# Performance work log

Hardware: AMD Instinct MI355X
Metric: run time of the kernel (lower is better)

## Reference

```python
import jax, jax.numpy as jnp
import numpy as np

B = 16
N = [4096, 1024, 256, 64, 16]
NF = [1, 16, 32, 64, 128, 256]
DEG = 6
KS = 5
LAT = 32


def spline_conv(x, edge_index, pseudo, W, root, bias):
    """SplineConv: open B-spline, degree 1, dim 3, kernel_size 5, sum aggregation (norm=False).
    x: [Nn, Cin], edge_index: [2, E] (src, dst), pseudo: [E, 3] in [0,1], W: [125, Cin, Cout]."""
    src, dst = edge_index[0], edge_index[1]
    v = pseudo * (KS - 1)                       # degree-1 open spline interval
    lo = jnp.clip(jnp.floor(v), 0.0, KS - 2)
    frac = v - lo                               # [E, 3]
    lo = lo.astype(jnp.int32)
    xs = x[src]                                 # [E, Cin] gather
    strides = jnp.array([1, KS, KS * KS], dtype=jnp.int32)
    msg = jnp.zeros((src.shape[0], W.shape[2]), dtype=x.dtype)
    for s in range(8):                          # (degree+1)^dim = 8 basis products
        bits = np.array([(s >> d) & 1 for d in range(3)], dtype=np.int32)
        basis = jnp.prod(jnp.where(bits[None, :] == 1, frac, 1.0 - frac), axis=1)  # [E]
        kidx = jnp.sum((lo + bits[None, :]) * strides[None, :], axis=1)            # [E]
        Wg = W[kidx]                                                               # [E, Cin, Cout]
        msg = msg + basis[:, None] * jnp.einsum('ei,eio->eo', xs, Wg)
    agg = jax.ops.segment_sum(msg, dst, num_segments=x.shape[0])
    return agg + x @ root + bias


def _fwd(fl, ei):
    (x, ea0, ea1, ea2, ea3, ea4, P01, P12, P23, P34, Pn1, P1n, P43, P32, P21, P10,
     W_c1, r_c1, b_c1, W_c2, r_c2, b_c2, W_c3, r_c3, b_c3, W_c4, r_c4, b_c4, W_c5, r_c5, b_c5,
     W_d5, r_d5, b_d5, W_d4, r_d4, b_d4, W_d3, r_d3, b_d3, W_d2, r_d2, b_d2, W_d1, r_d1, b_d1,
     fce1_w, fce1_b, fce21_w, fce21_b, fce22_w, fce22_b, fcd3_w, fcd3_b, fcd4_w, fcd4_b, eps) = fl
    ei0, ei1, ei2, ei3, ei4 = ei
    elu = jax.nn.elu
    # ---- encoder ----
    h = elu(spline_conv(x, ei0, ea0, W_c1, r_c1, b_c1))
    h = P01 @ h.reshape(B, N[0], NF[1])
    h = elu(spline_conv(h.reshape(-1, NF[1]), ei1, ea1, W_c2, r_c2, b_c2))
    h = P12 @ h.reshape(B, N[1], NF[2])
    h = elu(spline_conv(h.reshape(-1, NF[2]), ei2, ea2, W_c3, r_c3, b_c3))
    h = P23 @ h.reshape(B, N[2], NF[3])
    h = elu(spline_conv(h.reshape(-1, NF[3]), ei3, ea3, W_c4, r_c4, b_c4))
    h = P34 @ h.reshape(B, N[3], NF[4])
    h = elu(spline_conv(h.reshape(-1, NF[4]), ei4, ea4, W_c5, r_c5, b_c5))
    h = (Pn1 @ h.reshape(B, N[4], NF[5])).reshape(B, NF[5])
    # 1x1 convs over [B, C, 1, 1] == dense layers
    h = elu(h @ fce1_w + fce1_b)
    mu = h @ fce21_w + fce21_b
    logvar = h @ fce22_w + fce22_b
    # ---- reparameterize ----
    z = eps * jnp.exp(0.5 * logvar) + mu
    # ---- decoder ----
    h = elu(z @ fcd3_w + fcd3_b)
    h = elu(h @ fcd4_w + fcd4_b)
    h = P1n @ h.reshape(B, 1, NF[5])            # [B, N4, nf5]
    h = elu(spline_conv(h.reshape(-1, NF[5]), ei4, ea4, W_d5, r_d5, b_d5))
    h = P43 @ h.reshape(B, N[4], NF[4])
    h = elu(spline_conv(h.reshape(-1, NF[4]), ei3, ea3, W_d4, r_d4, b_d4))
    h = P32 @ h.reshape(B, N[3], NF[3])
    h = elu(spline_conv(h.reshape(-1, NF[3]), ei2, ea2, W_d3, r_d3, b_d3))
    h = P21 @ h.reshape(B, N[2], NF[2])
    h = elu(spline_conv(h.reshape(-1, NF[2]), ei1, ea1, W_d2, r_d2, b_d2))
    h = P10 @ h.reshape(B, N[1], NF[1])
    h = elu(spline_conv(h.reshape(-1, NF[1]), ei0, ea0, W_d1, r_d1, b_d1))
    recon = h.reshape(B, -1)                    # [B, N0] (nf0 == 1)
    return recon, mu, logvar


def setup_inputs() -> dict:
    key = jax.random.key(0)
    ks = iter(jax.random.split(key, 128))
    def nrm(shape, scale=1.0):
        return jax.random.normal(next(ks), shape, dtype=jnp.float32) * scale
    def edges(n):
        # per-sample random mesh-like connectivity, offset per graph copy
        e = jax.random.randint(next(ks), (2, B, n * DEG), 0, n)
        off = (jnp.arange(B) * n)[None, :, None]
        return (e + off).reshape(2, -1).astype(jnp.int32)
    inp = {}
    inp['x'] = nrm((B * N[0], NF[0]))
    for i in range(5):
        inp[f'ea{i}'] = jax.random.uniform(next(ks), (B * N[i] * DEG, 3), dtype=jnp.float32)
    pools = {'P01': (N[1], N[0]), 'P12': (N[2], N[1]), 'P23': (N[3], N[2]), 'P34': (N[4], N[3]),
             'Pn1': (1, N[4]), 'P1n': (N[4], 1), 'P43': (N[3], N[4]), 'P32': (N[2], N[3]),
             'P21': (N[1], N[2]), 'P10': (N[0], N[1])}
    for k2, (a, b) in pools.items():
        inp[k2] = nrm((a, b), 1.0 / np.sqrt(b))
    def spl(name, ci, co):
        inp[f'W_{name}'] = nrm((KS ** 3, ci, co), 0.1 / np.sqrt(ci))
        inp[f'r_{name}'] = nrm((ci, co), 1.0 / np.sqrt(ci))
        inp[f'b_{name}'] = nrm((co,), 0.01)
    spl('c1', NF[0], NF[1]); spl('c2', NF[1], NF[2]); spl('c3', NF[2], NF[3]); spl('c4', NF[3], NF[4]); spl('c5', NF[4], NF[5])
    spl('d5', NF[5], NF[4]); spl('d4', NF[4], NF[3]); spl('d3', NF[3], NF[2]); spl('d2', NF[2], NF[1]); spl('d1', NF[1], NF[0])
    def lin(name, ci, co):
        inp[f'{name}_w'] = nrm((ci, co), 1.0 / np.sqrt(ci))
        inp[f'{name}_b'] = nrm((co,), 0.01)
    lin('fce1', NF[5], NF[5]); lin('fce21', NF[5], LAT); lin('fce22', NF[5], LAT)
    lin('fcd3', LAT, NF[5]); lin('fcd4', NF[5], NF[5])
    inp['eps'] = nrm((B, LAT))
    for i in range(5):
        inp[f'ei{i}'] = edges(N[i])
    return inp


def reference(x, ea0, ea1, ea2, ea3, ea4, P01, P12, P23, P34, Pn1, P1n, P43, P32, P21, P10,
              W_c1, r_c1, b_c1, W_c2, r_c2, b_c2, W_c3, r_c3, b_c3, W_c4, r_c4, b_c4, W_c5, r_c5, b_c5,
              W_d5, r_d5, b_d5, W_d4, r_d4, b_d4, W_d3, r_d3, b_d3, W_d2, r_d2, b_d2, W_d1, r_d1, b_d1,
              fce1_w, fce1_b, fce21_w, fce21_b, fce22_w, fce22_b, fcd3_w, fcd3_b, fcd4_w, fcd4_b, eps,
              ei0, ei1, ei2, ei3, ei4):
    fl = (x, ea0, ea1, ea2, ea3, ea4, P01, P12, P23, P34, Pn1, P1n, P43, P32, P21, P10,
          W_c1, r_c1, b_c1, W_c2, r_c2, b_c2, W_c3, r_c3, b_c3, W_c4, r_c4, b_c4, W_c5, r_c5, b_c5,
          W_d5, r_d5, b_d5, W_d4, r_d4, b_d4, W_d3, r_d3, b_d3, W_d2, r_d2, b_d2, W_d1, r_d1, b_d1,
          fce1_w, fce1_b, fce21_w, fce21_b, fce22_w, fce22_b, fcd3_w, fcd3_b, fcd4_w, fcd4_b, eps)
    return _fwd(fl, (ei0, ei1, ei2, ei3, ei4))
```

## Files before the change

### kernel.cpp

```cpp
#include <hip/hip_runtime.h>
#include <hip/hip_bf16.h>

#define TPB 256
#define CDIV(a,b) (((a)+(b)-1)/(b))

__device__ __forceinline__ float elu_f(float v) {
    return v > 0.f ? v : expm1f(v);
}

__device__ __forceinline__ int ld_idx(const void* __restrict__ ei, int pos, int is64) {
    if (is64) return (int)((const long long*)ei)[pos];
    return ((const int*)ei)[pos];
}

__global__ void k_detect(const int* __restrict__ ei0_as_i32, int* __restrict__ flag) {
    if (threadIdx.x == 0 && blockIdx.x == 0) {
        int zeros = 0;
        for (int k = 0; k < 128; ++k)
            if (ei0_as_i32[2 * k + 1] == 0) zeros++;
        flag[0] = (zeros >= 120) ? 1 : 0;
    }
}

__global__ __launch_bounds__(TPB) void k_zero(float* __restrict__ p, int n) {
    int t = blockIdx.x * blockDim.x + threadIdx.x;
    if (t < n) p[t] = 0.f;
}

__global__ __launch_bounds__(TPB) void k_root(const float* __restrict__ x,
                                              const float* __restrict__ root,
                                              const float* __restrict__ bias,
                                              float* __restrict__ out,
                                              int nnode, int cin, int cout) {
    int t = blockIdx.x * blockDim.x + threadIdx.x;
    if (t >= nnode * cout) return;
    int n = t / cout, co = t - n * cout;
    const float* xp = x + n * cin;
    float acc = bias[co];
    for (int ci = 0; ci < cin; ++ci) acc = fmaf(xp[ci], root[ci * cout + co], acc);
    out[t] = acc;
}

__global__ __launch_bounds__(TPB) void k_root4(const float* __restrict__ x,
                                               const float* __restrict__ root,
                                               const float* __restrict__ bias,
                                               float* __restrict__ out,
                                               int nnode, int cin, int cout) {
    int t = blockIdx.x * blockDim.x + threadIdx.x;
    if (t >= nnode * cout) return;
    int n = t / cout, co = t - n * cout;
    const float4* xr = reinterpret_cast<const float4*>(x + n * cin);
    float a0 = 0.f, a1 = 0.f, a2 = 0.f, a3 = 0.f;
    int q4 = cin >> 2;
    for (int q = 0; q < q4; ++q) {
        float4 xv = xr[q];
        const float* rp = root + (q * 4) * cout + co;
        a0 = fmaf(xv.x, rp[0], a0);
        a1 = fmaf(xv.y, rp[cout], a1);
        a2 = fmaf(xv.z, rp[2 * cout], a2);
        a3 = fmaf(xv.w, rp[3 * cout], a3);
    }
    out[t] = bias[co] + ((a0 + a1) + (a2 + a3));
}

template <int CIN, int COUT, int CSPLIT>
__global__ __launch_bounds__(TPB) void k_msg4(const float* __restrict__ x,
                                              const float* __restrict__ pseudo,
                                              const void* __restrict__ ei,
                                              const float* __restrict__ W,
                                              float* __restrict__ agg, int E,
                                              const int* __restrict__ flag) {
    constexpr int COG = COUT / 4;
    constexpr int CPT = CIN / CSPLIT;
    int t = blockIdx.x * blockDim.x + threadIdx.x;
    if (t >= E * COG * CSPLIT) return;
    int is64 = flag[0];
    int cog = t % COG;
    int rest = t / COG;
    int cs = rest % CSPLIT;
    int e = rest / CSPLIT;
    int co0 = cog * 4;
    int src = ld_idx(ei, e, is64);
    int dst = ld_idx(ei, E + e, is64);

    float f[3]; int lo[3];
#pragma unroll
    for (int d = 0; d < 3; ++d) {
        float v = pseudo[e * 3 + d] * 4.f;
        float l = floorf(v);
        l = fminf(fmaxf(l, 0.f), 3.f);
        f[d] = v - l;
        lo[d] = (int)l;
    }
    float bas[8]; int wof[8];
#pragma unroll
    for (int s = 0; s < 8; ++s) {
        int b0 = s & 1, b1 = (s >> 1) & 1, b2 = (s >> 2) & 1;
        bas[s] = (b0 ? f[0] : 1.f - f[0]) * (b1 ? f[1] : 1.f - f[1]) * (b2 ? f[2] : 1.f - f[2]);
        int kidx = (lo[0] + b0) + 5 * (lo[1] + b1) + 25 * (lo[2] + b2);
        wof[s] = kidx * CIN * COUT + co0;
    }
    float a0 = 0.f, a1 = 0.f, a2 = 0.f, a3 = 0.f;
    const float* xp = x + src * CIN + cs * CPT;
    const int cbase = cs * CPT * COUT;
    for (int ci = 0; ci < CPT; ++ci) {
        float xv = xp[ci];
        int off = cbase + ci * COUT;
#pragma unroll
        for (int s = 0; s < 8; ++s) {
            float4 w = *reinterpret_cast<const float4*>(&W[wof[s] + off]);
            float bx = bas[s] * xv;
            a0 = fmaf(bx, w.x, a0);
            a1 = fmaf(bx, w.y, a1);
            a2 = fmaf(bx, w.z, a2);
            a3 = fmaf(bx, w.w, a3);
        }
    }
    float* ap = &agg[dst * COUT + co0];
    atomicAdd(ap + 0, a0);
    atomicAdd(ap + 1, a1);
    atomicAdd(ap + 2, a2);
    atomicAdd(ap + 3, a3);
}

template <int CIN, int COUT>
__global__ __launch_bounds__(TPB) void k_msg_s(const float* __restrict__ x,
                                               const float* __restrict__ pseudo,
                                               const void* __restrict__ ei,
                                               const float* __restrict__ W,
                                               float* __restrict__ agg, int E,
                                               const int* __restrict__ flag) {
    int t = blockIdx.x * blockDim.x + threadIdx.x;
    if (t >= E * COUT) return;
    int is64 = flag[0];
    int e = t / COUT, co = t - e * COUT;
    int src = ld_idx(ei, e, is64);
    int dst = ld_idx(ei, E + e, is64);
    float f[3]; int lo[3];
#pragma unroll
    for (int d = 0; d < 3; ++d) {
        float v = pseudo[e * 3 + d] * 4.f;
        float l = floorf(v);
        l = fminf(fmaxf(l, 0.f), 3.f);
        f[d] = v - l;
        lo[d] = (int)l;
    }
    float bas[8]; int wof[8];
#pragma unroll
    for (int s = 0; s < 8; ++s) {
        int b0 = s & 1, b1 = (s >> 1) & 1, b2 = (s >> 2) & 1;
        bas[s] = (b0 ? f[0] : 1.f - f[0]) * (b1 ? f[1] : 1.f - f[1]) * (b2 ? f[2] : 1.f - f[2]);
        int kidx = (lo[0] + b0) + 5 * (lo[1] + b1) + 25 * (lo[2] + b2);
        wof[s] = kidx * CIN * COUT + co;
    }
    float acc = 0.f;
    const float* xp = x + src * CIN;
    for (int ci = 0; ci < CIN; ++ci) {
        float xv = xp[ci];
#pragma unroll
        for (int s = 0; s < 8; ++s) acc = fmaf(bas[s] * xv, W[wof[s] + ci * COUT], acc);
    }
    atomicAdd(&agg[dst * COUT + co], acc);
}

template <int F, int JT, int ELU>
__global__ __launch_bounds__(TPB) void k_pool_t(const float* __restrict__ in,
                                                const float* __restrict__ P,
                                                float* __restrict__ out,
                                                int nout, int nin) {
    constexpr int FQ = F / 4;
    constexpr int IQ = TPB / FQ;
    constexpr int NI = 4;
    constexpr int TI = IQ * NI;
    __shared__ float4 s_in[JT * FQ];
    int fq = threadIdx.x % FQ;
    int iq = threadIdx.x / FQ;
    int b = blockIdx.y;
    int i0 = blockIdx.x * TI + iq * NI;
    int nchunk = nin / gridDim.z;
    int jbeg = blockIdx.z * nchunk;
    const float4* inb4 = reinterpret_cast<const float4*>(in + b * nin * F);

    float4 acc[NI];
#pragma unroll
    for (int n = 0; n < NI; ++n) acc[n] = make_float4(0.f, 0.f, 0.f, 0.f);

    for (int j0 = jbeg; j0 < jbeg + nchunk; j0 += JT) {
        __syncthreads();
        for (int t = threadIdx.x; t < JT * FQ; t += TPB) {
            float4 v = inb4[(j0 + t / FQ) * FQ + (t % FQ)];
            if (ELU) {
                v.x = elu_f(v.x); v.y = elu_f(v.y);
                v.z = elu_f(v.z); v.w = elu_f(v.w);
            }
            s_in[t] = v;
        }
        __syncthreads();
#pragma unroll 2
        for (int j = 0; j < JT; j += 4) {
            float4 v0 = s_in[(j + 0) * FQ + fq];
            float4 v1 = s_in[(j + 1) * FQ + fq];
            float4 v2 = s_in[(j + 2) * FQ + fq];
            float4 v3 = s_in[(j + 3) * FQ + fq];
#pragma unroll
            for (int n = 0; n < NI; ++n) {
                float4 pv = *reinterpret_cast<const float4*>(&P[(i0 + n) * nin + j0 + j]);
                acc[n].x = fmaf(pv.x, v0.x, acc[n].x); acc[n].y = fmaf(pv.x, v0.y, acc[n].y);
                acc[n].z = fmaf(pv.x, v0.z, acc[n].z); acc[n].w = fmaf(pv.x, v0.w, acc[n].w);
                acc[n].x = fmaf(pv.y, v1.x, acc[n].x); acc[n].y = fmaf(pv.y, v1.y, acc[n].y);
                acc[n].z = fmaf(pv.y, v1.z, acc[n].z); acc[n].w = fmaf(pv.y, v1.w, acc[n].w);
                acc[n].x = fmaf(pv.z, v2.x, acc[n].x); acc[n].y = fmaf(pv.z, v2.y, acc[n].y);
                acc[n].z = fmaf(pv.z, v2.z, acc[n].z); acc[n].w = fmaf(pv.z, v2.w, acc[n].w);
                acc[n].x = fmaf(pv.w, v3.x, acc[n].x); acc[n].y = fmaf(pv.w, v3.y, acc[n].y);
                acc[n].z = fmaf(pv.w, v3.z, acc[n].z); acc[n].w = fmaf(pv.w, v3.w, acc[n].w);
            }
        }
    }
#pragma unroll
    for (int n = 0; n < NI; ++n) {
        int i = i0 + n;
        if (i >= nout) continue;
        float* o = out + (b * nout + i) * F + fq * 4;
        if (gridDim.z > 1) {
            atomicAdd(o + 0, acc[n].x); atomicAdd(o + 1, acc[n].y);
            atomicAdd(o + 2, acc[n].z); atomicAdd(o + 3, acc[n].w);
        } else {
            *reinterpret_cast<float4*>(o) = acc[n];
        }
    }
}

__global__ __launch_bounds__(TPB) void k_pool_e(const float* __restrict__ in,
                                                const float* __restrict__ P,
                                                float* __restrict__ out,
                                                int nout, int nin, int F, int elu) {
    int t = blockIdx.x * blockDim.x + threadIdx.x;
    if (t >= 16 * nout * F) return;
    int f = t % F;
    int rest = t / F;
    int i = rest % nout;
    int b = rest / nout;
    const float* ip = in + b * nin * F + f;
    const float* pp = P + i * nin;
    float acc = 0.f;
    if (elu) {
#pragma unroll 4
        for (int j = 0; j < nin; ++j) acc = fmaf(pp[j], elu_f(ip[j * F]), acc);
    } else {
#pragma unroll 4
        for (int j = 0; j < nin; ++j) acc = fmaf(pp[j], ip[j * F], acc);
    }
    out[t] = acc;
}

__global__ __launch_bounds__(256) void k_fc_fused(
        const float* __restrict__ c5agg,
        const float* __restrict__ Pn1,
        const float* __restrict__ fce1_w, const float* __restrict__ fce1_b,
        const float* __restrict__ fce21_w, const float* __restrict__ fce21_b,
        const float* __restrict__ fce22_w, const float* __restrict__ fce22_b,
        const float* __restrict__ eps,
        const float* __restrict__ fcd3_w, const float* __restrict__ fcd3_b,
        const float* __restrict__ fcd4_w, const float* __restrict__ fcd4_b,
        const float* __restrict__ P1n,
        float* __restrict__ out_mu, float* __restrict__ out_lv,
        float* __restrict__ dec_in)
{
    __shared__ float s0[256], s1[256], s2[32];
    int b = blockIdx.x, t = threadIdx.x;

    const float* ap = c5agg + b * 4096 + t;
    float acc = 0.f;
#pragma unroll
    for (int n = 0; n < 16; ++n) acc = fmaf(Pn1[n], elu_f(ap[n * 256]), acc);
    s0[t] = acc;
    __syncthreads();

    float a = fce1_b[t];
    for (int ci = 0; ci < 256; ci += 8) {
#pragma unroll
        for (int k = 0; k < 8; ++k) a = fmaf(s0[ci + k], fce1_w[(ci + k) * 256 + t], a);
    }
    s1[t] = elu_f(a);
    __syncthreads();

    if (t < 64) {
        const float* w  = (t < 32) ? fce21_w : fce22_w;
        const float* bb = (t < 32) ? fce21_b : fce22_b;
        int co = t & 31;
        float m = bb[co];
        for (int ci = 0; ci < 256; ci += 8) {
#pragma unroll
            for (int k = 0; k < 8; ++k) m = fmaf(s1[ci + k], w[(ci + k) * 32 + co], m);
        }
        if (t < 32) { out_mu[b * 32 + co] = m; s2[co] = m; }
        else        { out_lv[b * 32 + co] = m; s0[co] = m; }
    }
    __syncthreads();
    if (t < 32) s2[t] = fmaf(eps[b * 32 + t], expf(0.5f * s0[t]), s2[t]);
    __syncthreads();

    float d = fcd3_b[t];
#pragma unroll
    for (int ci = 0; ci < 32; ++ci) d = fmaf(s2[ci], fcd3_w[ci * 256 + t], d);
    s0[t] = elu_f(d);
    __syncthreads();

    float e = fcd4_b[t];
    for (int ci = 0; ci < 256; ci += 8) {
#pragma unroll
        for (int k = 0; k < 8; ++k) e = fmaf(s0[ci + k], fcd4_w[(ci + k) * 256 + t], e);
    }
    e = elu_f(e);

    float* op = dec_in + b * 4096 + t;
#pragma unroll
    for (int n = 0; n < 16; ++n) op[n * 256] = P1n[n] * e;
}

__global__ __launch_bounds__(TPB) void k_elu_out(const float* __restrict__ in,
                                                 float* __restrict__ out, int n) {
    int t = blockIdx.x * blockDim.x + threadIdx.x;
    if (t < n) out[t] = elu_f(in[t]);
}

extern "C" void kernel_launch(void* const* d_in, const int* in_sizes, int n_in,
                              void* d_out, int out_size, void* d_ws, size_t ws_size,
                              hipStream_t stream) {
    const float* x    = (const float*)d_in[0];
    const float* ea0  = (const float*)d_in[1];
    const float* ea1  = (const float*)d_in[2];
    const float* ea2  = (const float*)d_in[3];
    const float* ea3  = (const float*)d_in[4];
    const float* ea4  = (const float*)d_in[5];
    const float* P01  = (const float*)d_in[6];
    const float* P12  = (const float*)d_in[7];
    const float* P23  = (const float*)d_in[8];
    const float* P34  = (const float*)d_in[9];
    const float* Pn1  = (const float*)d_in[10];
    const float* P1n  = (const float*)d_in[11];
    const float* P43  = (const float*)d_in[12];
    const float* P32  = (const float*)d_in[13];
    const float* P21  = (const float*)d_in[14];
    const float* P10  = (const float*)d_in[15];
    const float* W_c1 = (const float*)d_in[16]; const float* r_c1 = (const float*)d_in[17]; const float* b_c1 = (const float*)d_in[18];
    const float* W_c2 = (const float*)d_in[19]; const float* r_c2 = (const float*)d_in[20]; const float* b_c2 = (const float*)d_in[21];
    const float* W_c3 = (const float*)d_in[22]; const float* r_c3 = (const float*)d_in[23]; const float* b_c3 = (const float*)d_in[24];
    const float* W_c4 = (const float*)d_in[25]; const float* r_c4 = (const float*)d_in[26]; const float* b_c4 = (const float*)d_in[27];
    const float* W_c5 = (const float*)d_in[28]; const float* r_c5 = (const float*)d_in[29]; const float* b_c5 = (const float*)d_in[30];
    const float* W_d5 = (const float*)d_in[31]; const float* r_d5 = (const float*)d_in[32]; const float* b_d5 = (const float*)d_in[33];
    const float* W_d4 = (const float*)d_in[34]; const float* r_d4 = (const float*)d_in[35]; const float* b_d4 = (const float*)d_in[36];
    const float* W_d3 = (const float*)d_in[37]; const float* r_d3 = (const float*)d_in[38]; const float* b_d3 = (const float*)d_in[39];
    const float* W_d2 = (const float*)d_in[40]; const float* r_d2 = (const float*)d_in[41]; const float* b_d2 = (const float*)d_in[42];
    const float* W_d1 = (const float*)d_in[43]; const float* r_d1 = (const float*)d_in[44]; const float* b_d1 = (const float*)d_in[45];
    const float* fce1_w  = (const float*)d_in[46]; const float* fce1_b  = (const float*)d_in[47];
    const float* fce21_w = (const float*)d_in[48]; const float* fce21_b = (const float*)d_in[49];
    const float* fce22_w = (const float*)d_in[50]; const float* fce22_b = (const float*)d_in[51];
    const float* fcd3_w  = (const float*)d_in[52]; const float* fcd3_b  = (const float*)d_in[53];
    const float* fcd4_w  = (const float*)d_in[54]; const float* fcd4_b  = (const float*)d_in[55];
    const float* eps  = (const float*)d_in[56];
    const void* ei0 = d_in[57];
    const void* ei1 = d_in[58];
    const void* ei2 = d_in[59];
    const void* ei3 = d_in[60];
    const void* ei4 = d_in[61];

    const int E0 = 393216, E1 = 98304, E2 = 24576, E3 = 6144, E4 = 1536;
    const int N0 = 65536, N1 = 16384, N2 = 4096, N3 = 1024, N4 = 256;

    float* sm   = (float*)d_ws;
    float* bufA = sm + 13824;
    float* bufB = bufA + 1048576;
    int*  flag  = (int*)(bufB + 262144);

    float* out = (float*)d_out;
    float* out_mu = out + 65536;
    float* out_lv = out + 66048;

    auto g = [](int n) { return dim3((unsigned)CDIV(n, TPB)); };

    k_detect<<<1, 64, 0, stream>>>((const int*)ei0, flag);

    k_root<<<g(N0 * 16), TPB, 0, stream>>>(x, r_c1, b_c1, bufA, N0, 1, 16);
    k_msg4<1, 16, 1><<<g(E0 * 4), TPB, 0, stream>>>(x, ea0, ei0, W_c1, bufA, E0, flag);
    k_zero<<<g(262144), TPB, 0, stream>>>(bufB, 262144);
    k_pool_t<16, 128, 1><<<dim3(4, 16, 4), TPB, 0, stream>>>(bufA, P01, bufB, 1024, 4096);

    k_root4<<<g(N1 * 32), TPB, 0, stream>>>(bufB, r_c2, b_c2, bufA, N1, 16, 32);
    k_msg4<16, 32, 1><<<g(E1 * 8), TPB, 0, stream>>>(bufB, ea1, ei1, W_c2, bufA, E1, flag);
    k_zero<<<g(131072), TPB, 0, stream>>>(bufB, 131072);
    k_pool_t<32, 128, 1><<<dim3(2, 16, 4), TPB, 0, stream>>>(bufA, P12, bufB, 256, 1024);

    k_root4<<<g(N2 * 64), TPB, 0, stream>>>(bufB, r_c3, b_c3, bufA, N2, 32, 64);
    k_msg4<32, 64, 1><<<g(E2 * 16), TPB, 0, stream>>>(bufB, ea2, ei2, W_c3, bufA, E2, flag);
    k_zero<<<g(65536), TPB, 0, stream>>>(bufB, 65536);
    k_pool_t<64, 64, 1><<<dim3(1, 16, 2), TPB, 0, stream>>>(bufA, P23, bufB, 64, 256);

    k_root4<<<g(N3 * 128), TPB, 0, stream>>>(bufB, r_c4, b_c4, bufA, N3, 64, 128);
    k_msg4<64, 128, 1><<<g(E3 * 32), TPB, 0, stream>>>(bufB, ea3, ei3, W_c4, bufA, E3, flag);
    k_pool_e<<<g(16 * 16 * 128), TPB, 0, stream>>>(bufA, P34, bufB, 16, 64, 128, 1);

    k_root4<<<g(N4 * 256), TPB, 0, stream>>>(bufB, r_c5, b_c5, bufA, N4, 128, 256);
    k_msg4<128, 256, 2><<<g(E4 * 128), TPB, 0, stream>>>(bufB, ea4, ei4, W_c5, bufA, E4, flag);

    k_fc_fused<<<16, 256, 0, stream>>>(bufA, Pn1,
                                       fce1_w, fce1_b, fce21_w, fce21_b, fce22_w, fce22_b,
                                       eps, fcd3_w, fcd3_b, fcd4_w, fcd4_b, P1n,
                                       out_mu, out_lv, bufA);

    k_root4<<<g(N4 * 128), TPB, 0, stream>>>(bufA, r_d5, b_d5, bufB, N4, 256, 128);
    k_msg4<256, 128, 4><<<g(E4 * 128), TPB, 0, stream>>>(bufA, ea4, ei4, W_d5, bufB, E4, flag);
    k_pool_e<<<g(16 * 64 * 128), TPB, 0, stream>>>(bufB, P43, bufA, 64, 16, 128, 1);

    k_root4<<<g(N3 * 64), TPB, 0, stream>>>(bufA, r_d4, b_d4, bufB, N3, 128, 64);
    k_msg4<128, 64, 2><<<g(E3 * 32), TPB, 0, stream>>>(bufA, ea3, ei3, W_d4, bufB, E3, flag);
    k_pool_t<64, 64, 1><<<dim3(4, 16, 1), TPB, 0, stream>>>(bufB, P32, bufA, 256, 64);

    k_root4<<<g(N2 * 32), TPB, 0, stream>>>(bufA, r_d3, b_d3, bufB, N2, 64, 32);
    k_msg4<64, 32, 1><<<g(E2 * 8), TPB, 0, stream>>>(bufA, ea2, ei2, W_d3, bufB, E2, flag);
    k_zero<<<g(524288), TPB, 0, stream>>>(bufA, 524288);
    k_pool_t<32, 128, 1><<<dim3(8, 16, 2), TPB, 0, stream>>>(bufB, P21, bufA, 1024, 256);

    k_root4<<<g(N1 * 16), TPB, 0, stream>>>(bufA, r_d2, b_d2, bufB, N1, 32, 16);
    k_msg4<32, 16, 1><<<g(E1 * 4), TPB, 0, stream>>>(bufA, ea1, ei1, W_d2, bufB, E1, flag);
    k_pool_t<16, 128, 1><<<dim3(16, 16, 1), TPB, 0, stream>>>(bufB, P10, bufA, 4096, 1024);

    k_root4<<<g(N0 * 1), TPB, 0, stream>>>(bufA, r_d1, b_d1, bufB, N0, 16, 1);
    k_msg_s<16, 1><<<g(E0 * 1), TPB, 0, stream>>>(bufA, ea0, ei0, W_d1, bufB, E0, flag);
    k_elu_out<<<g(N0), TPB, 0, stream>>>(bufB, out, 65536);
}
```

Before: 1.062 ms.

## Specialize first/last spline convs with shared-memory aggregation and rework pooling and FC kernels

The first encoder conv is replaced by a per-graph kernel that fuses the root/bias term and aggregates messages with shared-memory atomics, using weights cached in LDS. The last decoder conv does the same, writing per-segment partial sums that a finalize kernel reduces together with ELU. The pooling kernels become non-atomic one-output-per-thread GEMVs, which removes the zeroing launches, with an optional split-K path and a reduction step. The FC block moves to 1024 threads with split-K partial sums. Together these cut global atomics, launches and serialized FC work, but they depend on edges being grouped per graph and on a larger workspace being available.

```diff
diff --git a/kernel.cpp b/kernel.cpp
--- a/kernel.cpp
+++ b/kernel.cpp
@@ -11,6 +11,25 @@
 __device__ __forceinline__ int ld_idx(const void* __restrict__ ei, int pos, int is64) {
     if (is64) return (int)((const long long*)ei)[pos];
     return ((const int*)ei)[pos];
+}
+
+__device__ __forceinline__ void spline_basis(const float* __restrict__ pseudo, int e,
+                                             float bas[8], int kidx[8]) {
+    float f[3]; int lo[3];
+#pragma unroll
+    for (int d = 0; d < 3; ++d) {
+        float v = pseudo[e * 3 + d] * 4.f;
+        float l = floorf(v);
+        l = fminf(fmaxf(l, 0.f), 3.f);
+        f[d] = v - l;
+        lo[d] = (int)l;
+    }
+#pragma unroll
+    for (int s = 0; s < 8; ++s) {
+        int b0 = s & 1, b1 = (s >> 1) & 1, b2 = (s >> 2) & 1;
+        bas[s] = (b0 ? f[0] : 1.f - f[0]) * (b1 ? f[1] : 1.f - f[1]) * (b2 ? f[2] : 1.f - f[2]);
+        kidx[s] = (lo[0] + b0) + 5 * (lo[1] + b1) + 25 * (lo[2] + b2);
+    }
 }
 
 __global__ void k_detect(const int* __restrict__ ei0_as_i32, int* __restrict__ flag) {
@@ -25,20 +44,6 @@
 __global__ __launch_bounds__(TPB) void k_zero(float* __restrict__ p, int n) {
     int t = blockIdx.x * blockDim.x + threadIdx.x;
     if (t < n) p[t] = 0.f;
-}
-
-__global__ __launch_bounds__(TPB) void k_root(const float* __restrict__ x,
-                                              const float* __restrict__ root,
-                                              const float* __restrict__ bias,
-                                              float* __restrict__ out,
-                                              int nnode, int cin, int cout) {
-    int t = blockIdx.x * blockDim.x + threadIdx.x;
-    if (t >= nnode * cout) return;
-    int n = t / cout, co = t - n * cout;
-    const float* xp = x + n * cin;
-    float acc = bias[co];
-    for (int ci = 0; ci < cin; ++ci) acc = fmaf(xp[ci], root[ci * cout + co], acc);
-    out[t] = acc;
 }
 
 __global__ __launch_bounds__(TPB) void k_root4(const float* __restrict__ x,
@@ -82,24 +87,11 @@
     int co0 = cog * 4;
     int src = ld_idx(ei, e, is64);
     int dst = ld_idx(ei, E + e, is64);
-
-    float f[3]; int lo[3];
-#pragma unroll
-    for (int d = 0; d < 3; ++d) {
-        float v = pseudo[e * 3 + d] * 4.f;
-        float l = floorf(v);
-        l = fminf(fmaxf(l, 0.f), 3.f);
-        f[d] = v - l;
-        lo[d] = (int)l;
-    }
-    float bas[8]; int wof[8];
-#pragma unroll
-    for (int s = 0; s < 8; ++s) {
-        int b0 = s & 1, b1 = (s >> 1) & 1, b2 = (s >> 2) & 1;
-        bas[s] = (b0 ? f[0] : 1.f - f[0]) * (b1 ? f[1] : 1.f - f[1]) * (b2 ? f[2] : 1.f - f[2]);
-        int kidx = (lo[0] + b0) + 5 * (lo[1] + b1) + 25 * (lo[2] + b2);
-        wof[s] = kidx * CIN * COUT + co0;
-    }
+    float bas[8]; int kidx[8];
+    spline_basis(pseudo, e, bas, kidx);
+    int wof[8];
+#pragma unroll
+    for (int s = 0; s < 8; ++s) wof[s] = kidx[s] * CIN * COUT + co0;
     float a0 = 0.f, a1 = 0.f, a2 = 0.f, a3 = 0.f;
     const float* xp = x + src * CIN + cs * CPT;
     const int cbase = cs * CPT * COUT;
@@ -136,31 +128,176 @@
     int e = t / COUT, co = t - e * COUT;
     int src = ld_idx(ei, e, is64);
     int dst = ld_idx(ei, E + e, is64);
-    float f[3]; int lo[3];
-#pragma unroll
-    for (int d = 0; d < 3; ++d) {
-        float v = pseudo[e * 3 + d] * 4.f;
-        float l = floorf(v);
-        l = fminf(fmaxf(l, 0.f), 3.f);
-        f[d] = v - l;
-        lo[d] = (int)l;
-    }
-    float bas[8]; int wof[8];
-#pragma unroll
-    for (int s = 0; s < 8; ++s) {
-        int b0 = s & 1, b1 = (s >> 1) & 1, b2 = (s >> 2) & 1;
-        bas[s] = (b0 ? f[0] : 1.f - f[0]) * (b1 ? f[1] : 1.f - f[1]) * (b2 ? f[2] : 1.f - f[2]);
-        int kidx = (lo[0] + b0) + 5 * (lo[1] + b1) + 25 * (lo[2] + b2);
-        wof[s] = kidx * CIN * COUT + co;
-    }
+    float bas[8]; int kidx[8];
+    spline_basis(pseudo, e, bas, kidx);
     float acc = 0.f;
     const float* xp = x + src * CIN;
     for (int ci = 0; ci < CIN; ++ci) {
         float xv = xp[ci];
 #pragma unroll
-        for (int s = 0; s < 8; ++s) acc = fmaf(bas[s] * xv, W[wof[s] + ci * COUT], acc);
+        for (int s = 0; s < 8; ++s)
+            acc = fmaf(bas[s] * xv, W[kidx[s] * CIN * COUT + ci * COUT + co], acc);
     }
     atomicAdd(&agg[dst * COUT + co], acc);
+}
+
+__global__ __launch_bounds__(1024) void k_msg_c1(const float* __restrict__ x,
+                                                 const float* __restrict__ pseudo,
+                                                 const void* __restrict__ ei,
+                                                 const float* __restrict__ W,
+                                                 const float* __restrict__ root,
+                                                 const float* __restrict__ bias,
+                                                 float* __restrict__ agg,
+                                                 const int* __restrict__ flag) {
+    __shared__ float s_acc[4096 * 4];
+    __shared__ float s_w[125 * 4];
+    int b = blockIdx.x, cg = blockIdx.y, t = threadIdx.x;
+    int co0 = cg * 4;
+    int is64 = flag[0];
+    if (t < 500) s_w[t] = W[(t >> 2) * 16 + co0 + (t & 3)];
+    float r0 = root[co0], r1 = root[co0 + 1], r2 = root[co0 + 2], r3 = root[co0 + 3];
+    float b0 = bias[co0], b1 = bias[co0 + 1], b2 = bias[co0 + 2], b3 = bias[co0 + 3];
+    for (int n = t; n < 4096; n += 1024) {
+        float xv = x[b * 4096 + n];
+        s_acc[n * 4 + 0] = fmaf(xv, r0, b0);
+        s_acc[n * 4 + 1] = fmaf(xv, r1, b1);
+        s_acc[n * 4 + 2] = fmaf(xv, r2, b2);
+        s_acc[n * 4 + 3] = fmaf(xv, r3, b3);
+    }
+    __syncthreads();
+    int ebeg = b * 24576;
+    for (int k = t; k < 24576; k += 1024) {
+        int e = ebeg + k;
+        int src = ld_idx(ei, e, is64);
+        int dst = ld_idx(ei, 393216 + e, is64);
+        float xv = x[src];
+        float bas[8]; int kidx[8];
+        spline_basis(pseudo, e, bas, kidx);
+        float m0 = 0.f, m1 = 0.f, m2 = 0.f, m3 = 0.f;
+#pragma unroll
+        for (int s = 0; s < 8; ++s) {
+            const float* wp = s_w + kidx[s] * 4;
+            float bs = bas[s];
+            m0 = fmaf(bs, wp[0], m0);
+            m1 = fmaf(bs, wp[1], m1);
+            m2 = fmaf(bs, wp[2], m2);
+            m3 = fmaf(bs, wp[3], m3);
+        }
+        int dl = (dst - b * 4096) * 4;
+        atomicAdd(&s_acc[dl + 0], m0 * xv);
+        atomicAdd(&s_acc[dl + 1], m1 * xv);
+        atomicAdd(&s_acc[dl + 2], m2 * xv);
+        atomicAdd(&s_acc[dl + 3], m3 * xv);
+    }
+    __syncthreads();
+    for (int n = t; n < 4096; n += 1024) {
+        float4 v = *reinterpret_cast<float4*>(&s_acc[n * 4]);
+        *reinterpret_cast<float4*>(&agg[(b * 4096 + n) * 16 + co0]) = v;
+    }
+}
+
+__global__ __launch_bounds__(512) void k_msg_d1(const float* __restrict__ x,
+                                                const float* __restrict__ pseudo,
+                                                const void* __restrict__ ei,
+                                                const float* __restrict__ W,
+                                                float* __restrict__ part,
+                                                const int* __restrict__ flag) {
+    __shared__ float s_acc[4096];
+    __shared__ float s_w[2000];
+    int b = blockIdx.x, seg = blockIdx.y, t = threadIdx.x;
+    int is64 = flag[0];
+    for (int i = t; i < 2000; i += 512) s_w[i] = W[i];
+    for (int n = t; n < 4096; n += 512) s_acc[n] = 0.f;
+    __syncthreads();
+    int ebeg = b * 24576 + seg * 3072;
+    for (int k = t; k < 3072; k += 512) {
+        int e = ebeg + k;
+        int src = ld_idx(ei, e, is64);
+        int dst = ld_idx(ei, 393216 + e, is64);
+        float bas[8]; int kidx[8];
+        spline_basis(pseudo, e, bas, kidx);
+        const float* xp = x + src * 16;
+        float m = 0.f;
+#pragma unroll
+        for (int s = 0; s < 8; ++s) {
+            const float* wp = s_w + kidx[s] * 16;
+            float p = 0.f;
+#pragma unroll
+            for (int ci = 0; ci < 16; ++ci) p = fmaf(xp[ci], wp[ci], p);
+            m = fmaf(bas[s], p, m);
+        }
+        atomicAdd(&s_acc[dst - b * 4096], m);
+    }
+    __syncthreads();
+    for (int n = t; n < 4096; n += 512) part[(b * 8 + seg) * 4096 + n] = s_acc[n];
+}
+
+__global__ __launch_bounds__(TPB) void k_d1_fin(const float* __restrict__ root,
+                                                const float* __restrict__ part,
+                                                float* __restrict__ out) {
+    int t = blockIdx.x * blockDim.x + threadIdx.x;
+    if (t >= 65536) return;
+    int b = t >> 12, n = t & 4095;
+    float a = root[t];
+#pragma unroll
+    for (int s = 0; s < 8; ++s) a += part[(b * 8 + s) * 4096 + n];
+    out[t] = elu_f(a);
+}
+
+template <int F, int ELU>
+__global__ __launch_bounds__(256) void k_poolg(const float* __restrict__ in,
+                                               const float* __restrict__ P,
+                                               float* __restrict__ out,
+                                               int nout, int nin) {
+    constexpr int FQ = F / 4;
+    constexpr int TI = 256 / FQ;
+    constexpr int JT = 128;
+    __shared__ float4 s_in[JT * FQ];
+    int fq = threadIdx.x % FQ;
+    int i = threadIdx.x / FQ;
+    int b = blockIdx.y;
+    int gi = blockIdx.x * TI + i;
+    int nchunk = nin / gridDim.z;
+    int jbeg = blockIdx.z * nchunk;
+    const float4* inb4 = reinterpret_cast<const float4*>(in + b * nin * F);
+    const float* prow = P + gi * nin;
+    float4 acc = make_float4(0.f, 0.f, 0.f, 0.f);
+    for (int j0 = jbeg; j0 < jbeg + nchunk; j0 += JT) {
+        __syncthreads();
+        for (int t = threadIdx.x; t < JT * FQ; t += 256) {
+            float4 v = inb4[(j0 + t / FQ) * FQ + (t % FQ)];
+            if (ELU) {
+                v.x = elu_f(v.x); v.y = elu_f(v.y);
+                v.z = elu_f(v.z); v.w = elu_f(v.w);
+            }
+            s_in[t] = v;
+        }
+        __syncthreads();
+#pragma unroll 4
+        for (int j = 0; j < JT; j += 4) {
+            float4 pv = *reinterpret_cast<const float4*>(prow + j0 + j);
+            float4 v0 = s_in[(j + 0) * FQ + fq];
+            float4 v1 = s_in[(j + 1) * FQ + fq];
+            float4 v2 = s_in[(j + 2) * FQ + fq];
+            float4 v3 = s_in[(j + 3) * FQ + fq];
+            acc.x = fmaf(pv.x, v0.x, acc.x); acc.y = fmaf(pv.x, v0.y, acc.y);
+            acc.z = fmaf(pv.x, v0.z, acc.z); acc.w = fmaf(pv.x, v0.w, acc.w);
+            acc.x = fmaf(pv.y, v1.x, acc.x); acc.y = fmaf(pv.y, v1.y, acc.y);
+            acc.z = fmaf(pv.y, v1.z, acc.z); acc.w = fmaf(pv.y, v1.w, acc.w);
+            acc.x = fmaf(pv.z, v2.x, acc.x); acc.y = fmaf(pv.z, v2.y, acc.y);
+            acc.z = fmaf(pv.z, v2.z, acc.z); acc.w = fmaf(pv.z, v2.w, acc.w);
+            acc.x = fmaf(pv.w, v3.x, acc.x); acc.y = fmaf(pv.w, v3.y, acc.y);
+            acc.z = fmaf(pv.w, v3.z, acc.z); acc.w = fmaf(pv.w, v3.w, acc.w);
+        }
+    }
+    float* o = out + (((size_t)blockIdx.z * 16 + b) * nout + gi) * F + fq * 4;
+    *reinterpret_cast<float4*>(o) = acc;
+}
+
+__global__ __launch_bounds__(TPB) void k_reduce2(const float* __restrict__ part,
+                                                 float* __restrict__ out, int n) {
+    int t = blockIdx.x * blockDim.x + threadIdx.x;
+    if (t < n) out[t] = part[t] + part[t + n];
 }
 
 template <int F, int JT, int ELU>
@@ -180,11 +317,9 @@
     int nchunk = nin / gridDim.z;
     int jbeg = blockIdx.z * nchunk;
     const float4* inb4 = reinterpret_cast<const float4*>(in + b * nin * F);
-
     float4 acc[NI];
 #pragma unroll
     for (int n = 0; n < NI; ++n) acc[n] = make_float4(0.f, 0.f, 0.f, 0.f);
-
     for (int j0 = jbeg; j0 < jbeg + nchunk; j0 += JT) {
         __syncthreads();
         for (int t = threadIdx.x; t < JT * FQ; t += TPB) {
@@ -253,9 +388,8 @@
     out[t] = acc;
 }
 
-__global__ __launch_bounds__(256) void k_fc_fused(
-        const float* __restrict__ c5agg,
-        const float* __restrict__ Pn1,
+__global__ __launch_bounds__(1024) void k_fc_fused2(
+        const float* __restrict__ c5agg, const float* __restrict__ Pn1,
         const float* __restrict__ fce1_w, const float* __restrict__ fce1_b,
         const float* __restrict__ fce21_w, const float* __restrict__ fce21_b,
         const float* __restrict__ fce22_w, const float* __restrict__ fce22_b,
@@ -264,58 +398,82 @@
         const float* __restrict__ fcd4_w, const float* __restrict__ fcd4_b,
         const float* __restrict__ P1n,
         float* __restrict__ out_mu, float* __restrict__ out_lv,
-        float* __restrict__ dec_in)
-{
-    __shared__ float s0[256], s1[256], s2[32];
+        float* __restrict__ dec_in) {
+    __shared__ float s0[256], s1[256], sz[32], sp[1024];
     int b = blockIdx.x, t = threadIdx.x;
-
-    const float* ap = c5agg + b * 4096 + t;
-    float acc = 0.f;
-#pragma unroll
-    for (int n = 0; n < 16; ++n) acc = fmaf(Pn1[n], elu_f(ap[n * 256]), acc);
-    s0[t] = acc;
-    __syncthreads();
-
-    float a = fce1_b[t];
-    for (int ci = 0; ci < 256; ci += 8) {
-#pragma unroll
-        for (int k = 0; k < 8; ++k) a = fmaf(s0[ci + k], fce1_w[(ci + k) * 256 + t], a);
-    }
-    s1[t] = elu_f(a);
-    __syncthreads();
-
+    if (t < 256) {
+        const float* ap = c5agg + b * 4096 + t;
+        float acc = 0.f;
+#pragma unroll
+        for (int n = 0; n < 16; ++n) acc = fmaf(Pn1[n], elu_f(ap[n * 256]), acc);
+        s0[t] = acc;
+    }
+    __syncthreads();
+    {
+        int q = t >> 8, co = t & 255;
+        const float* w = fce1_w + co;
+        float a = 0.f;
+        int c0 = q * 64;
+        for (int ci = 0; ci < 64; ci += 8) {
+#pragma unroll
+            for (int k = 0; k < 8; ++k) a = fmaf(s0[c0 + ci + k], w[(c0 + ci + k) * 256], a);
+        }
+        sp[t] = a;
+    }
+    __syncthreads();
+    if (t < 256) s1[t] = elu_f(sp[t] + sp[t + 256] + sp[t + 512] + sp[t + 768] + fce1_b[t]);
+    __syncthreads();
+    if (t < 512) {
+        int which = t >> 8, r = t & 255;
+        int co = r & 31, q = r >> 5;
+        const float* w = (which ? fce22_w : fce21_w) + co;
+        float a = 0.f;
+        int c0 = q * 32;
+#pragma unroll
+        for (int k = 0; k < 32; ++k) a = fmaf(s1[c0 + k], w[(c0 + k) * 32], a);
+        sp[t] = a;
+    }
+    __syncthreads();
     if (t < 64) {
-        const float* w  = (t < 32) ? fce21_w : fce22_w;
-        const float* bb = (t < 32) ? fce21_b : fce22_b;
-        int co = t & 31;
-        float m = bb[co];
-        for (int ci = 0; ci < 256; ci += 8) {
-#pragma unroll
-            for (int k = 0; k < 8; ++k) m = fmaf(s1[ci + k], w[(ci + k) * 32 + co], m);
-        }
-        if (t < 32) { out_mu[b * 32 + co] = m; s2[co] = m; }
-        else        { out_lv[b * 32 + co] = m; s0[co] = m; }
-    }
-    __syncthreads();
-    if (t < 32) s2[t] = fmaf(eps[b * 32 + t], expf(0.5f * s0[t]), s2[t]);
-    __syncthreads();
-
-    float d = fcd3_b[t];
-#pragma unroll
-    for (int ci = 0; ci < 32; ++ci) d = fmaf(s2[ci], fcd3_w[ci * 256 + t], d);
-    s0[t] = elu_f(d);
-    __syncthreads();
-
-    float e = fcd4_b[t];
-    for (int ci = 0; ci < 256; ci += 8) {
-#pragma unroll
-        for (int k = 0; k < 8; ++k) e = fmaf(s0[ci + k], fcd4_w[(ci + k) * 256 + t], e);
-    }
-    e = elu_f(e);
-
-    float* op = dec_in + b * 4096 + t;
-#pragma unroll
-    for (int n = 0; n < 16; ++n) op[n * 256] = P1n[n] * e;
+        int which = t >> 5, co = t & 31;
+        float m = (which ? fce22_b : fce21_b)[co];
+        int base = which * 256 + co;
+#pragma unroll
+        for (int q = 0; q < 8; ++q) m += sp[base + q * 32];
+        if (which == 0) { out_mu[b * 32 + co] = m; s0[co] = m; }
+        else            { out_lv[b * 32 + co] = m; s0[64 + co] = m; }
+    }
+    __syncthreads();
+    if (t < 32) sz[t] = fmaf(eps[b * 32 + t], expf(0.5f * s0[64 + t]), s0[t]);
+    __syncthreads();
+    if (t < 256) {
+        float d = fcd3_b[t];
+#pragma unroll
+        for (int ci = 0; ci < 32; ++ci) d = fmaf(sz[ci], fcd3_w[ci * 256 + t], d);
+        s0[t] = elu_f(d);
+    }
+    __syncthreads();
+    {
+        int q = t >> 8, co = t & 255;
+        const float* w = fcd4_w + co;
+        float a = 0.f;
+        int c0 = q * 64;
+        for (int ci = 0; ci < 64; ci += 8) {
+#pragma unroll
+            for (int k = 0; k < 8; ++k) a = fmaf(s0[c0 + ci + k], w[(c0 + ci + k) * 256], a);
+        }
+        sp[t] = a;
+    }
+    __syncthreads();
+    if (t < 256) s1[t] = elu_f(sp[t] + sp[t + 256] + sp[t + 512] + sp[t + 768] + fcd4_b[t]);
+    __syncthreads();
+    {
+        float* op = dec_in + b * 4096;
+        for (int idx = t; idx < 4096; idx += 1024) {
+            int n = idx >> 8, f = idx & 255;
+            op[idx] = P1n[n] * s1[f];
+        }
+    }
 }
 
 __global__ __launch_bounds__(TPB) void k_elu_out(const float* __restrict__ in,
@@ -365,13 +523,16 @@
     const void* ei3 = d_in[60];
     const void* ei4 = d_in[61];
 
-    const int E0 = 393216, E1 = 98304, E2 = 24576, E3 = 6144, E4 = 1536;
+    const int E1 = 98304, E2 = 24576, E3 = 6144, E4 = 1536;
     const int N0 = 65536, N1 = 16384, N2 = 4096, N3 = 1024, N4 = 256;
 
     float* sm   = (float*)d_ws;
     float* bufA = sm + 13824;
     float* bufB = bufA + 1048576;
     int*  flag  = (int*)(bufB + 262144);
+    float* part = bufB + 262144 + 64;
+    const size_t WS_NEED = (size_t)(13824 + 1048576 + 262144 + 64 + 524288) * 4;
+    const bool big_ws = ws_size >= WS_NEED;
 
     float* out = (float*)d_out;
     float* out_mu = out + 65536;
@@ -381,15 +542,17 @@
 
     k_detect<<<1, 64, 0, stream>>>((const int*)ei0, flag);
 
-    k_root<<<g(N0 * 16), TPB, 0, stream>>>(x, r_c1, b_c1, bufA, N0, 1, 16);
-    k_msg4<1, 16, 1><<<g(E0 * 4), TPB, 0, stream>>>(x, ea0, ei0, W_c1, bufA, E0, flag);
-    k_zero<<<g(262144), TPB, 0, stream>>>(bufB, 262144);
-    k_pool_t<16, 128, 1><<<dim3(4, 16, 4), TPB, 0, stream>>>(bufA, P01, bufB, 1024, 4096);
+    k_msg_c1<<<dim3(16, 4), 1024, 0, stream>>>(x, ea0, ei0, W_c1, r_c1, b_c1, bufA, flag);
+    if (big_ws) {
+        k_poolg<16, 1><<<dim3(16, 16, 2), 256, 0, stream>>>(bufA, P01, part, 1024, 4096);
+        k_reduce2<<<g(262144), TPB, 0, stream>>>(part, bufB, 262144);
+    } else {
+        k_poolg<16, 1><<<dim3(16, 16, 1), 256, 0, stream>>>(bufA, P01, bufB, 1024, 4096);
+    }
 
     k_root4<<<g(N1 * 32), TPB, 0, stream>>>(bufB, r_c2, b_c2, bufA, N1, 16, 32);
     k_msg4<16, 32, 1><<<g(E1 * 8), TPB, 0, stream>>>(bufB, ea1, ei1, W_c2, bufA, E1, flag);
-    k_zero<<<g(131072), TPB, 0, stream>>>(bufB, 131072);
-    k_pool_t<32, 128, 1><<<dim3(2, 16, 4), TPB, 0, stream>>>(bufA, P12, bufB, 256, 1024);
+    k_poolg<32, 1><<<dim3(8, 16, 1), 256, 0, stream>>>(bufA, P12, bufB, 256, 1024);
 
     k_root4<<<g(N2 * 64), TPB, 0, stream>>>(bufB, r_c3, b_c3, bufA, N2, 32, 64);
     k_msg4<32, 64, 1><<<g(E2 * 16), TPB, 0, stream>>>(bufB, ea2, ei2, W_c3, bufA, E2, flag);
@@ -403,10 +566,10 @@
     k_root4<<<g(N4 * 256), TPB, 0, stream>>>(bufB, r_c5, b_c5, bufA, N4, 128, 256);
     k_msg4<128, 256, 2><<<g(E4 * 128), TPB, 0, stream>>>(bufB, ea4, ei4, W_c5, bufA, E4, flag);
 
-    k_fc_fused<<<16, 256, 0, stream>>>(bufA, Pn1,
-                                       fce1_w, fce1_b, fce21_w, fce21_b, fce22_w, fce22_b,
-                                       eps, fcd3_w, fcd3_b, fcd4_w, fcd4_b, P1n,
-                                       out_mu, out_lv, bufA);
+    k_fc_fused2<<<16, 1024, 0, stream>>>(bufA, Pn1,
+                                         fce1_w, fce1_b, fce21_w, fce21_b, fce22_w, fce22_b,
+                                         eps, fcd3_w, fcd3_b, fcd4_w, fcd4_b, P1n,
+                                         out_mu, out_lv, bufA);
 
     k_root4<<<g(N4 * 128), TPB, 0, stream>>>(bufA, r_d5, b_d5, bufB, N4, 256, 128);
     k_msg4<256, 128, 4><<<g(E4 * 128), TPB, 0, stream>>>(bufA, ea4, ei4, W_d5, bufB, E4, flag);
@@ -418,14 +581,18 @@
 
     k_root4<<<g(N2 * 32), TPB, 0, stream>>>(bufA, r_d3, b_d3, bufB, N2, 64, 32);
     k_msg4<64, 32, 1><<<g(E2 * 8), TPB, 0, stream>>>(bufA, ea2, ei2, W_d3, bufB, E2, flag);
-    k_zero<<<g(524288), TPB, 0, stream>>>(bufA, 524288);
-    k_pool_t<32, 128, 1><<<dim3(8, 16, 2), TPB, 0, stream>>>(bufB, P21, bufA, 1024, 256);
+    k_poolg<32, 1><<<dim3(32, 16, 1), 256, 0, stream>>>(bufB, P21, bufA, 1024, 256);
 
     k_root4<<<g(N1 * 16), TPB, 0, stream>>>(bufA, r_d2, b_d2, bufB, N1, 32, 16);
     k_msg4<32, 16, 1><<<g(E1 * 4), TPB, 0, stream>>>(bufA, ea1, ei1, W_d2, bufB, E1, flag);
-    k_pool_t<16, 128, 1><<<dim3(16, 16, 1), TPB, 0, stream>>>(bufB, P10, bufA, 4096, 1024);
+    k_poolg<16, 1><<<dim3(64, 16, 1), 256, 0, stream>>>(bufB, P10, bufA, 4096, 1024);
 
     k_root4<<<g(N0 * 1), TPB, 0, stream>>>(bufA, r_d1, b_d1, bufB, N0, 16, 1);
-    k_msg_s<16, 1><<<g(E0 * 1), TPB, 0, stream>>>(bufA, ea0, ei0, W_d1, bufB, E0, flag);
-    k_elu_out<<<g(N0), TPB, 0, stream>>>(bufB, out, 65536);
-}
+    if (big_ws) {
+        k_msg_d1<<<dim3(16, 8), 512, 0, stream>>>(bufA, ea0, ei0, W_d1, part, flag);
+        k_d1_fin<<<g(65536), TPB, 0, stream>>>(bufB, part, out);
+    } else {
+        k_msg_s<16, 1><<<g(393216), TPB, 0, stream>>>(bufA, ea0, ei0, W_d1, bufB, 393216, flag);
+        k_elu_out<<<g(N0), TPB, 0, stream>>>(bufB, out, 65536);
+    }
+}
```

Result: faster. 1.021 ms (-3.9%).
